# Optimization experiments

Hardware: AMD Instinct MI355X
Metric: run time of the kernel (lower is better)

The kernel has to match this reference:

```python
import jax, jax.numpy as jnp
import numpy as np

NEG_SLOPE = 0.2  # PyG GATConv default negative_slope


def gat_conv(x, edge_index, W, att_src, att_dst, bias):
    """PyG-style GATConv (concat heads, add_self_loops=True, eval mode).
    x: [N, F_in], edge_index: [2, E] (row 0 = src j, row 1 = dst i).
    W: [F_in, H*C], att_src/att_dst: [H, C], bias: [H*C].
    """
    N = x.shape[0]
    H, C = att_src.shape
    loops = jnp.arange(N, dtype=edge_index.dtype)
    src = jnp.concatenate([edge_index[0], loops])  # [E+N]
    dst = jnp.concatenate([edge_index[1], loops])
    h = (x @ W).reshape(N, H, C)                              # [N,H,C]
    a_src = jnp.einsum('nhc,hc->nh', h, att_src)              # [N,H]
    a_dst = jnp.einsum('nhc,hc->nh', h, att_dst)
    alpha = jax.nn.leaky_relu(a_src[src] + a_dst[dst], NEG_SLOPE)  # [E+N,H]
    # segment softmax over edges sharing the same destination node
    m = jax.ops.segment_max(alpha, dst, num_segments=N)       # [N,H]
    e = jnp.exp(alpha - jax.lax.stop_gradient(m)[dst])
    denom = jax.ops.segment_sum(e, dst, num_segments=N)       # [N,H]
    a = e / (denom[dst] + 1e-16)                              # [E+N,H]
    msg = h[src] * a[:, :, None]                              # [E+N,H,C]
    out = jax.ops.segment_sum(msg, dst, num_segments=N)       # [N,H,C]
    return out.reshape(N, H * C) + bias


def setup_inputs() -> dict:
    key = jax.random.key(0)
    ks = jax.random.split(key, 10)
    N, F, NC, C1, H1 = 50000, 128, 40, 16, 8
    E = 800000
    x = jax.random.normal(ks[0], (N, F), dtype=jnp.float32)
    edge_index = jax.random.randint(ks[1], (2, E), 0, N, dtype=jnp.int64)
    s1 = 1.0 / np.sqrt(F)
    W1 = jax.random.uniform(ks[2], (F, H1 * C1), jnp.float32, -s1, s1)
    att_src1 = jax.random.uniform(ks[3], (H1, C1), jnp.float32, -1.0, 1.0) * s1
    att_dst1 = jax.random.uniform(ks[4], (H1, C1), jnp.float32, -1.0, 1.0) * s1
    bias1 = jnp.zeros((H1 * C1,), jnp.float32)
    s2 = 1.0 / np.sqrt(H1 * C1)
    W2 = jax.random.uniform(ks[5], (H1 * C1, NC), jnp.float32, -s2, s2)
    att_src2 = jax.random.uniform(ks[6], (1, NC), jnp.float32, -1.0, 1.0) * s2
    att_dst2 = jax.random.uniform(ks[7], (1, NC), jnp.float32, -1.0, 1.0) * s2
    bias2 = jnp.zeros((NC,), jnp.float32)
    return {"x": x, "edge_index": edge_index, "W1": W1, "att_src1": att_src1,
            "att_dst1": att_dst1, "bias1": bias1, "W2": W2, "att_src2": att_src2,
            "att_dst2": att_dst2, "bias2": bias2}


def reference(x, edge_index, W1, att_src1, att_dst1, bias1, W2, att_src2, att_dst2, bias2):
    h = gat_conv(x, edge_index, W1, att_src1, att_dst1, bias1)   # [N, 128]
    # dropout in eval mode = identity
    out = gat_conv(h, edge_index, W2, att_src2, att_dst2, bias2)  # [N, 40]
    return out
```

## Files before the change

kernel.cpp:

```cpp
#include <hip/hip_runtime.h>
#include <hip/hip_bf16.h>
#include <math.h>

#define NEG_SLOPE 0.2f

typedef __bf16 bf16x8 __attribute__((ext_vector_type(8)));
typedef float f32x4 __attribute__((ext_vector_type(4)));

__device__ __forceinline__ float lrelu(float x) { return x > 0.f ? x : NEG_SLOPE * x; }

__device__ __forceinline__ unsigned short f2bfu(float f) {
    unsigned int ua = __float_as_uint(f);
    return (unsigned short)((ua + 0x7fffu + ((ua >> 16) & 1u)) >> 16);
}
__device__ __forceinline__ float bfu2f(unsigned short u) {
    return __uint_as_float(((unsigned int)u) << 16);
}
__device__ __forceinline__ float bf_lo(unsigned int u) { return __uint_as_float(u << 16); }
__device__ __forceinline__ float bf_hi(unsigned int u) { return __uint_as_float(u & 0xffff0000u); }

__global__ __launch_bounds__(256) void k_hist(const int* __restrict__ ei, int E, int N,
                                              int* __restrict__ cnt, int* __restrict__ rank) {
    int e = blockIdx.x * 256 + threadIdx.x;
    if (e >= E + N) return;
    int d = (e < E) ? ei[E + e] : (e - E);
    rank[e] = atomicAdd(&cnt[d], 1);
}

__global__ __launch_bounds__(256) void k_scan_part(const int* __restrict__ cnt, int N,
                                                   int* __restrict__ psum) {
    __shared__ int sh[256];
    int t = threadIdx.x;
    int base = blockIdx.x * 1024 + t * 4;
    int tl = 0;
#pragma unroll
    for (int j = 0; j < 4; ++j) tl += (base + j < N) ? cnt[base + j] : 0;
    sh[t] = tl; __syncthreads();
    for (int off = 128; off > 0; off >>= 1) {
        if (t < off) sh[t] += sh[t + off];
        __syncthreads();
    }
    if (t == 0) psum[blockIdx.x] = sh[0];
}

__global__ __launch_bounds__(256) void k_scan_mid(int* __restrict__ psum, int nb) {
    __shared__ int sh[256];
    int t = threadIdx.x;
    int v = (t < nb) ? psum[t] : 0;
    sh[t] = v; __syncthreads();
    for (int off = 1; off < 256; off <<= 1) {
        int a = (t >= off) ? sh[t - off] : 0;
        __syncthreads();
        sh[t] += a;
        __syncthreads();
    }
    psum[t] = sh[t] - v;
}

__global__ __launch_bounds__(256) void k_scan_add(const int* __restrict__ cnt, int N,
                                                  const int* __restrict__ psum,
                                                  int* __restrict__ rowptr) {
    __shared__ int sh[256];
    int t = threadIdx.x;
    int base = blockIdx.x * 1024 + t * 4;
    int c[4]; int tl = 0;
#pragma unroll
    for (int j = 0; j < 4; ++j) { c[j] = (base + j < N) ? cnt[base + j] : 0; tl += c[j]; }
    sh[t] = tl; __syncthreads();
    for (int off = 1; off < 256; off <<= 1) {
        int a = (t >= off) ? sh[t - off] : 0;
        __syncthreads();
        sh[t] += a;
        __syncthreads();
    }
    int run = psum[blockIdx.x] + (sh[t] - tl);
#pragma unroll
    for (int j = 0; j < 4; ++j) {
        if (base + j < N) { rowptr[base + j] = run; run += c[j]; }
    }
}

__global__ __launch_bounds__(256) void k_scatter(const int* __restrict__ ei, int E, int N,
                                                 const int* __restrict__ rowptr,
                                                 const int* __restrict__ rank,
                                                 int* __restrict__ col) {
    int e = blockIdx.x * 256 + threadIdx.x;
    if (e >= E + N) return;
    int s, d;
    if (e < E) { s = ei[e]; d = ei[E + e]; } else { s = d = e - E; }
    col[rowptr[d] + rank[e]] = s;
}

__global__ __launch_bounds__(256) void k_wpack(const float* __restrict__ W,
                                               bf16x8* __restrict__ Wp) {
    int idx = blockIdx.x * 256 + threadIdx.x;
    if (idx >= 2048) return;
    int n = idx & 15, quad = (idx >> 4) & 3, c = (idx >> 6) & 3, ct = idx >> 8;
    bf16x8 v;
#pragma unroll
    for (int j = 0; j < 8; ++j)
        v[j] = (__bf16)W[(c * 32 + quad * 8 + j) * 128 + ct * 16 + n];
    Wp[idx] = v;
}

__global__ __launch_bounds__(256) void k_wpack2(const float* __restrict__ W2,
                                                bf16x8* __restrict__ W2p) {
    int idx = blockIdx.x * 256 + threadIdx.x;
    if (idx >= 768) return;
    int n = idx & 15, quad = (idx >> 4) & 3, c = (idx >> 6) & 3, ct = idx >> 8;
    int colc = ct * 16 + n;
    bf16x8 v;
#pragma unroll
    for (int j = 0; j < 8; ++j)
        v[j] = (colc < 40) ? (__bf16)W2[(c * 32 + quad * 8 + j) * 40 + colc] : (__bf16)0.f;
    W2p[idx] = v;
}

__global__ __launch_bounds__(256) void k_gemm1(const float* __restrict__ x,
                                               const bf16x8* __restrict__ Wp,
                                               const float* __restrict__ att_s,
                                               const float* __restrict__ att_d,
                                               unsigned short* __restrict__ h1A,
                                               unsigned short* __restrict__ h1B,
                                               float* __restrict__ a_src,
                                               float* __restrict__ a_dst, int N) {
    int t = threadIdx.x;
    int w = t >> 6, lane = t & 63, quad = lane >> 4, n16 = lane & 15;
    int row0 = blockIdx.x * 64 + w * 16;
    int arow = row0 + n16; if (arow >= N) arow = N - 1;
    const float* px = x + (size_t)arow * 128;

    bf16x8 ah[4], al[4];
#pragma unroll
    for (int c = 0; c < 4; ++c) {
        float4 v0 = *(const float4*)&px[c * 32 + quad * 8];
        float4 v1 = *(const float4*)&px[c * 32 + quad * 8 + 4];
        float xf[8] = {v0.x, v0.y, v0.z, v0.w, v1.x, v1.y, v1.z, v1.w};
#pragma unroll
        for (int j = 0; j < 8; ++j) {
            __bf16 hi = (__bf16)xf[j];
            ah[c][j] = hi;
            al[c][j] = (__bf16)(xf[j] - (float)hi);
        }
    }

    f32x4 acc[8];
#pragma unroll
    for (int ct = 0; ct < 8; ++ct) acc[ct] = (f32x4){0.f, 0.f, 0.f, 0.f};

    const uint4* wp4 = (const uint4*)Wp;
#pragma unroll
    for (int ct = 0; ct < 8; ++ct) {
#pragma unroll
        for (int c = 0; c < 4; ++c) {
            union { uint4 u; bf16x8 b; } bu;
            bu.u = wp4[((ct * 4 + c) * 4 + quad) * 16 + n16];
            acc[ct] = __builtin_amdgcn_mfma_f32_16x16x32_bf16(ah[c], bu.b, acc[ct], 0, 0, 0);
            acc[ct] = __builtin_amdgcn_mfma_f32_16x16x32_bf16(al[c], bu.b, acc[ct], 0, 0, 0);
        }
    }

    float asv[8], adv[8];
#pragma unroll
    for (int ct = 0; ct < 8; ++ct) {
        asv[ct] = att_s[ct * 16 + n16];
        adv[ct] = att_d[ct * 16 + n16];
    }
    int nodeb = row0 + quad * 4;
#pragma unroll
    for (int ct = 0; ct < 8; ++ct) {
        unsigned short* hp = (ct < 4) ? h1A : h1B;
        int chl = (ct & 3) * 16 + n16;
#pragma unroll
        for (int reg = 0; reg < 4; ++reg) {
            int node = nodeb + reg;
            float hv = acc[ct][reg];
            float ps = hv * asv[ct];
            float pd = hv * adv[ct];
#pragma unroll
            for (int m = 1; m < 16; m <<= 1) {
                ps += __shfl_xor(ps, m);
                pd += __shfl_xor(pd, m);
            }
            if (node < N) {
                hp[(size_t)node * 64 + chl] = f2bfu(hv);
                if (n16 == 0) {
                    a_src[(size_t)node * 8 + ct] = ps;
                    a_dst[(size_t)node * 8 + ct] = pd;
                }
            }
        }
    }
}

__global__ __launch_bounds__(256) void k_aggr1(const int* __restrict__ rowptr,
                                               const int* __restrict__ cnt,
                                               const int* __restrict__ col,
                                               const float* __restrict__ a_src,
                                               const float* __restrict__ a_dst,
                                               const unsigned int* __restrict__ hp,
                                               const float* __restrict__ bias1,
                                               unsigned int* __restrict__ out1h,
                                               unsigned int* __restrict__ out1l, int N, int p) {
    __shared__ float evs[4][2][128];
    __shared__ int   cls[4][2][32];
    int t = threadIdx.x;
    int w = t >> 6;
    int lane = t & 63;
    int half = lane >> 5;
    int u = lane & 31;
    int node = blockIdx.x * 8 + w * 2 + half;
    bool nv = (node < N);
    int nodec = nv ? node : (N - 1);
    int beg = rowptr[nodec];
    int deg = nv ? cnt[nodec] : 0;
    int degO = __shfl_xor(deg, 32);
    int degmax = (deg > degO) ? deg : degO;
    if (degmax <= 0) return;

    int hh = u >> 3;
    float4 ad4 = *(const float4*)&a_dst[(size_t)nodec * 8 + p * 4];

    float* myev = &evs[w][half][0];
    int*   mycl = &cls[w][half][0];

    float den = 0.f, n0 = 0.f, n1 = 0.f;
    int c = 0;
    while (c < degmax) {
        int slot = c + u;
        int slotc = (slot < deg) ? slot : (deg - 1);
        if (slotc < 0) slotc = 0;
        int su = col[beg + slotc];
        float4 as4 = *(const float4*)&a_src[(size_t)su * 8 + p * 4];
        bool valid = (slot < deg);
        float e0 = valid ? __expf(lrelu(as4.x + ad4.x)) : 0.f;
        float e1 = valid ? __expf(lrelu(as4.y + ad4.y)) : 0.f;
        float e2 = valid ? __expf(lrelu(as4.z + ad4.z)) : 0.f;
        float e3 = valid ? __expf(lrelu(as4.w + ad4.w)) : 0.f;
        *(float4*)&myev[u * 4] = make_float4(e0, e1, e2, e3);
        mycl[u] = su;

        int ccm = degmax - c; ccm = (ccm < 32) ? ccm : 32;
        int sP = mycl[0];
        unsigned int uP = hp[sP * 32 + u];
        for (int i = 0; i < ccm; ++i) {
            int in = (i + 1 < ccm) ? (i + 1) : i;
            int sN = mycl[in];
            unsigned int uN = hp[sN * 32 + u];
            float ev = myev[i * 4 + hh];
            den += ev;
            n0 = fmaf(ev, bf_lo(uP), n0);
            n1 = fmaf(ev, bf_hi(uP), n1);
            uP = uN;
        }
        c += 32;
    }
    if (nv) {
        float inv = 1.f / (den + 1e-16f);
        int ch = p * 64 + 2 * u;
        float2 b = *(const float2*)&bias1[ch];
        float o0 = fmaf(n0, inv, b.x), o1 = fmaf(n1, inv, b.y);
        unsigned short h0 = f2bfu(o0), h1 = f2bfu(o1);
        float l0 = o0 - bfu2f(h0), l1 = o1 - bfu2f(h1);
        size_t idx = (size_t)node * 64 + p * 32 + u;
        out1h[idx] = (unsigned int)h0 | ((unsigned int)h1 << 16);
        out1l[idx] = (unsigned int)f2bfu(l0) | ((unsigned int)f2bfu(l1) << 16);
    }
}

__global__ __launch_bounds__(256) void k_gemm2(const unsigned int* __restrict__ out1h,
                                               const unsigned int* __restrict__ out1l,
                                               const bf16x8* __restrict__ W2p,
                                               const float* __restrict__ att_s2,
                                               const float* __restrict__ att_d2,
                                               unsigned short* __restrict__ h2s,
                                               float* __restrict__ a_src2,
                                               float* __restrict__ a_dst2, int N) {
    int t = threadIdx.x;
    int w = t >> 6, lane = t & 63, quad = lane >> 4, n16 = lane & 15;
    int row0 = blockIdx.x * 64 + w * 16;
    int arow = row0 + n16; if (arow >= N) arow = N - 1;

    bf16x8 ah[4], al[4];
#pragma unroll
    for (int c = 0; c < 4; ++c) {
        size_t base = (size_t)arow * 64 + (c * 32 + quad * 8) / 2;
        union { uint4 u; bf16x8 b; } hu, lu;
        hu.u = *(const uint4*)&out1h[base];
        lu.u = *(const uint4*)&out1l[base];
        ah[c] = hu.b;
        al[c] = lu.b;
    }

    f32x4 acc[3];
#pragma unroll
    for (int ct = 0; ct < 3; ++ct) acc[ct] = (f32x4){0.f, 0.f, 0.f, 0.f};

    const uint4* wp4 = (const uint4*)W2p;
#pragma unroll
    for (int ct = 0; ct < 3; ++ct) {
#pragma unroll
        for (int c = 0; c < 4; ++c) {
            union { uint4 u; bf16x8 b; } bu;
            bu.u = wp4[((ct * 4 + c) * 4 + quad) * 16 + n16];
            acc[ct] = __builtin_amdgcn_mfma_f32_16x16x32_bf16(ah[c], bu.b, acc[ct], 0, 0, 0);
            acc[ct] = __builtin_amdgcn_mfma_f32_16x16x32_bf16(al[c], bu.b, acc[ct], 0, 0, 0);
        }
    }

    float asv[3], adv[3];
#pragma unroll
    for (int ct = 0; ct < 3; ++ct) {
        int ch = ct * 16 + n16;
        asv[ct] = (ch < 40) ? att_s2[ch] : 0.f;
        adv[ct] = (ch < 40) ? att_d2[ch] : 0.f;
    }
    int nodeb = row0 + quad * 4;
#pragma unroll
    for (int reg = 0; reg < 4; ++reg) {
        int node = nodeb + reg;
        float ps = 0.f, pd = 0.f;
#pragma unroll
        for (int ct = 0; ct < 3; ++ct) {
            float hv = acc[ct][reg];
            ps = fmaf(hv, asv[ct], ps);
            pd = fmaf(hv, adv[ct], pd);
            int ch = ct * 16 + n16;
            if (node < N && ch < 40) h2s[(size_t)node * 40 + ch] = f2bfu(hv);
        }
#pragma unroll
        for (int m = 1; m < 16; m <<= 1) {
            ps += __shfl_xor(ps, m);
            pd += __shfl_xor(pd, m);
        }
        if (node < N && n16 == 0) {
            a_src2[node] = ps;
            a_dst2[node] = pd;
        }
    }
}

__global__ __launch_bounds__(256) void k_aggr2(const int* __restrict__ rowptr,
                                               const int* __restrict__ cnt,
                                               const int* __restrict__ col,
                                               const float* __restrict__ a_src,
                                               const float* __restrict__ a_dst,
                                               const unsigned int* __restrict__ h2b,
                                               const float* __restrict__ bias2,
                                               float* __restrict__ out, int N) {
    __shared__ float evs[4][2][32];
    __shared__ int   cls[4][2][32];
    int t = threadIdx.x;
    int w = t >> 6;
    int lane = t & 63;
    int half = lane >> 5;
    int u = lane & 31;
    int node = blockIdx.x * 8 + w * 2 + half;
    bool nv = (node < N);
    int nodec = nv ? node : (N - 1);
    int beg = rowptr[nodec];
    int deg = nv ? cnt[nodec] : 0;
    int degO = __shfl_xor(deg, 32);
    int degmax = (deg > degO) ? deg : degO;
    if (degmax <= 0) return;

    int ucl = (u < 20) ? u : 19;
    float ad = a_dst[nodec];
    float* myev = &evs[w][half][0];
    int*   mycl = &cls[w][half][0];

    float den = 0.f, a0 = 0.f, a1 = 0.f;
    int c = 0;
    while (c < degmax) {
        int slot = c + u;
        int slotc = (slot < deg) ? slot : (deg - 1);
        if (slotc < 0) slotc = 0;
        int su = col[beg + slotc];
        float ev = (slot < deg) ? __expf(lrelu(a_src[su] + ad)) : 0.f;
        myev[u] = ev;
        mycl[u] = su;

        int ccm = degmax - c; ccm = (ccm < 32) ? ccm : 32;
        int sP = mycl[0];
        unsigned int uP = h2b[sP * 20 + ucl];
        for (int i = 0; i < ccm; ++i) {
            int in = (i + 1 < ccm) ? (i + 1) : i;
            int sN = mycl[in];
            unsigned int uN = h2b[sN * 20 + ucl];
            float evv = myev[i];
            den += evv;
            a0 = fmaf(evv, bf_lo(uP), a0);
            a1 = fmaf(evv, bf_hi(uP), a1);
            uP = uN;
        }
        c += 32;
    }
    if (nv && u < 20) {
        float inv = 1.f / (den + 1e-16f);
        float2 b = *(const float2*)&bias2[2 * u];
        float2 o = make_float2(fmaf(a0, inv, b.x), fmaf(a1, inv, b.y));
        *(float2*)&out[(size_t)node * 40 + 2 * u] = o;
    }
}

extern "C" void kernel_launch(void* const* d_in, const int* in_sizes, int n_in,
                              void* d_out, int out_size, void* d_ws, size_t ws_size,
                              hipStream_t stream) {
    const float* x   = (const float*)d_in[0];
    const int*   ei  = (const int*)d_in[1];
    const float* W1  = (const float*)d_in[2];
    const float* as1 = (const float*)d_in[3];
    const float* ad1 = (const float*)d_in[4];
    const float* b1  = (const float*)d_in[5];
    const float* W2  = (const float*)d_in[6];
    const float* as2 = (const float*)d_in[7];
    const float* ad2 = (const float*)d_in[8];
    const float* b2  = (const float*)d_in[9];

    int N = in_sizes[0] / 128;
    int E = in_sizes[1] / 2;
    int EN = E + N;
    size_t Np = (size_t)((N + 3) & ~3);
    size_t ENp = ((size_t)EN + 3) & ~3;

    float* ws = (float*)d_ws;
    unsigned int* out1h = (unsigned int*)ws; ws += Np * 64;
    unsigned int* out1l = (unsigned int*)ws; ws += Np * 64;
    unsigned int* h1A = (unsigned int*)ws; ws += Np * 32;
    unsigned int* h1Bp = (unsigned int*)ws; ws += Np * 32;
    unsigned int* h2b = (unsigned int*)ws; ws += Np * 20;
    float* a_src1  = ws; ws += Np * 8;
    float* a_dst1  = ws; ws += Np * 8;
    float* a_src2v = ws; ws += Np;
    float* a_dst2v = ws; ws += Np;
    bf16x8* Wp  = (bf16x8*)ws; ws += 2048 * 4;
    bf16x8* W2p = (bf16x8*)ws; ws += 768 * 4;
    int* cnt    = (int*)ws; ws += Np;
    int* rowptr = (int*)ws; ws += Np;
    int* psum   = (int*)ws; ws += 256;
    int* col    = (int*)ws; ws += ENp;
    int* rank   = (int*)ws; ws += ENp;

    int nb = (N + 1023) / 1024;

    hipMemsetAsync(cnt, 0, (size_t)N * sizeof(int), stream);
    k_wpack<<<8, 256, 0, stream>>>(W1, Wp);
    k_wpack2<<<3, 256, 0, stream>>>(W2, W2p);
    k_hist<<<(EN + 255) / 256, 256, 0, stream>>>(ei, E, N, cnt, rank);
    k_scan_part<<<nb, 256, 0, stream>>>(cnt, N, psum);
    k_scan_mid<<<1, 256, 0, stream>>>(psum, nb);
    k_scan_add<<<nb, 256, 0, stream>>>(cnt, N, psum, rowptr);
    k_scatter<<<(EN + 255) / 256, 256, 0, stream>>>(ei, E, N, rowptr, rank, col);

    k_gemm1<<<(N + 63) / 64, 256, 0, stream>>>(x, Wp, as1, ad1,
                                               (unsigned short*)h1A, (unsigned short*)h1Bp,
                                               a_src1, a_dst1, N);
    int nag = (N + 7) / 8;
    k_aggr1<<<nag, 256, 0, stream>>>(rowptr, cnt, col, a_src1, a_dst1, h1A, b1, out1h, out1l, N, 0);
    k_aggr1<<<nag, 256, 0, stream>>>(rowptr, cnt, col, a_src1, a_dst1, h1Bp, b1, out1h, out1l, N, 1);
    k_gemm2<<<(N + 63) / 64, 256, 0, stream>>>(out1h, out1l, W2p, as2, ad2,
                                               (unsigned short*)h2b, a_src2v, a_dst2v, N);
    k_aggr2<<<nag, 256, 0, stream>>>(rowptr, cnt, col, a_src2v, a_dst2v, h2b, b2, (float*)d_out, N);
}
```

Before: 249.4 us.

## Split layer-1 aggregation into four head-pair passes and use 16-bit edge indices

The layer-1 features and source attention scores are stored as four slices of two heads each, 32 channels per slice. Aggregation then runs four passes, each with 16 lanes per destination node instead of two passes with 32 lanes. This shrinks the randomly gathered per-pass working set so it is more likely to stay in cache. The CSR column and rank arrays become 16-bit, halving index traffic, but this only works while the node count and per-node degree stay below 65536. It also adds extra launches and re-reads of the edge list per pass.

```diff
diff --git a/kernel.cpp b/kernel.cpp
--- a/kernel.cpp
+++ b/kernel.cpp
@@ -20,11 +20,12 @@
 __device__ __forceinline__ float bf_hi(unsigned int u) { return __uint_as_float(u & 0xffff0000u); }
 
 __global__ __launch_bounds__(256) void k_hist(const int* __restrict__ ei, int E, int N,
-                                              int* __restrict__ cnt, int* __restrict__ rank) {
+                                              int* __restrict__ cnt,
+                                              unsigned short* __restrict__ rank) {
     int e = blockIdx.x * 256 + threadIdx.x;
     if (e >= E + N) return;
     int d = (e < E) ? ei[E + e] : (e - E);
-    rank[e] = atomicAdd(&cnt[d], 1);
+    rank[e] = (unsigned short)atomicAdd(&cnt[d], 1);
 }
 
 __global__ __launch_bounds__(256) void k_scan_part(const int* __restrict__ cnt, int N,
@@ -82,13 +83,13 @@
 
 __global__ __launch_bounds__(256) void k_scatter(const int* __restrict__ ei, int E, int N,
                                                  const int* __restrict__ rowptr,
-                                                 const int* __restrict__ rank,
-                                                 int* __restrict__ col) {
+                                                 const unsigned short* __restrict__ rank,
+                                                 unsigned short* __restrict__ col) {
     int e = blockIdx.x * 256 + threadIdx.x;
     if (e >= E + N) return;
     int s, d;
     if (e < E) { s = ei[e]; d = ei[E + e]; } else { s = d = e - E; }
-    col[rowptr[d] + rank[e]] = s;
+    col[rowptr[d] + (int)rank[e]] = (unsigned short)s;
 }
 
 __global__ __launch_bounds__(256) void k_wpack(const float* __restrict__ W,
@@ -120,9 +121,8 @@
                                                const bf16x8* __restrict__ Wp,
                                                const float* __restrict__ att_s,
                                                const float* __restrict__ att_d,
-                                               unsigned short* __restrict__ h1A,
-                                               unsigned short* __restrict__ h1B,
-                                               float* __restrict__ a_src,
+                                               unsigned short* __restrict__ h1q, size_t qstride,
+                                               float* __restrict__ a_srcq, size_t astride,
                                                float* __restrict__ a_dst, int N) {
     int t = threadIdx.x;
     int w = t >> 6, lane = t & 63, quad = lane >> 4, n16 = lane & 15;
@@ -169,8 +169,9 @@
     int nodeb = row0 + quad * 4;
 #pragma unroll
     for (int ct = 0; ct < 8; ++ct) {
-        unsigned short* hp = (ct < 4) ? h1A : h1B;
-        int chl = (ct & 3) * 16 + n16;
+        int q = ct >> 1, hsel = ct & 1;
+        unsigned short* hp = h1q + (size_t)q * qstride;
+        int chl = hsel * 16 + n16;
 #pragma unroll
         for (int reg = 0; reg < 4; ++reg) {
             int node = nodeb + reg;
@@ -183,9 +184,9 @@
                 pd += __shfl_xor(pd, m);
             }
             if (node < N) {
-                hp[(size_t)node * 64 + chl] = f2bfu(hv);
+                hp[(size_t)node * 32 + chl] = f2bfu(hv);
                 if (n16 == 0) {
-                    a_src[(size_t)node * 8 + ct] = ps;
+                    a_srcq[(size_t)q * astride + node * 2 + hsel] = ps;
                     a_dst[(size_t)node * 8 + ct] = pd;
                 }
             }
@@ -195,14 +196,160 @@
 
 __global__ __launch_bounds__(256) void k_aggr1(const int* __restrict__ rowptr,
                                                const int* __restrict__ cnt,
-                                               const int* __restrict__ col,
-                                               const float* __restrict__ a_src,
+                                               const unsigned short* __restrict__ col,
+                                               const float* __restrict__ a_srcq,
                                                const float* __restrict__ a_dst,
                                                const unsigned int* __restrict__ hp,
                                                const float* __restrict__ bias1,
                                                unsigned int* __restrict__ out1h,
-                                               unsigned int* __restrict__ out1l, int N, int p) {
-    __shared__ float evs[4][2][128];
+                                               unsigned int* __restrict__ out1l, int N, int q) {
+    __shared__ float evs[4][4][32];
+    __shared__ int   cls[4][4][16];
+    int t = threadIdx.x;
+    int w = t >> 6;
+    int lane = t & 63;
+    int sub = lane >> 4;
+    int u = lane & 15;
+    int node = blockIdx.x * 16 + w * 4 + sub;
+    bool nv = (node < N);
+    int nodec = nv ? node : (N - 1);
+    int beg = rowptr[nodec];
+    int deg = nv ? cnt[nodec] : 0;
+    int m1 = deg, mo;
+    mo = __shfl_xor(m1, 16); m1 = (m1 > mo) ? m1 : mo;
+    mo = __shfl_xor(m1, 32); m1 = (m1 > mo) ? m1 : mo;
+    int degmax = m1;
+    if (degmax <= 0) return;
+
+    int hsel = u >> 3;
+    float2 ad2 = *(const float2*)&a_dst[(size_t)nodec * 8 + q * 2];
+
+    float* myev = &evs[w][sub][0];
+    int*   mycl = &cls[w][sub][0];
+
+    float den = 0.f, n0 = 0.f, n1 = 0.f;
+    int c = 0;
+    while (c < degmax) {
+        int slot = c + u;
+        int slotc = (slot < deg) ? slot : (deg - 1);
+        if (slotc < 0) slotc = 0;
+        int su = (int)col[beg + slotc];
+        float2 as2 = *(const float2*)&a_srcq[(size_t)su * 2];
+        bool valid = (slot < deg);
+        float e0 = valid ? __expf(lrelu(as2.x + ad2.x)) : 0.f;
+        float e1 = valid ? __expf(lrelu(as2.y + ad2.y)) : 0.f;
+        *(float2*)&myev[u * 2] = make_float2(e0, e1);
+        mycl[u] = su;
+
+        int ccm = degmax - c; ccm = (ccm < 16) ? ccm : 16;
+        int sP = mycl[0];
+        unsigned int uP = hp[sP * 16 + u];
+        for (int i = 0; i < ccm; ++i) {
+            int in = (i + 1 < ccm) ? (i + 1) : i;
+            int sN = mycl[in];
+            unsigned int uN = hp[sN * 16 + u];
+            float ev = myev[i * 2 + hsel];
+            den += ev;
+            n0 = fmaf(ev, bf_lo(uP), n0);
+            n1 = fmaf(ev, bf_hi(uP), n1);
+            uP = uN;
+        }
+        c += 16;
+    }
+    if (nv) {
+        float inv = 1.f / (den + 1e-16f);
+        int ch = q * 32 + 2 * u;
+        float2 b = *(const float2*)&bias1[ch];
+        float o0 = fmaf(n0, inv, b.x), o1 = fmaf(n1, inv, b.y);
+        unsigned short h0 = f2bfu(o0), h1 = f2bfu(o1);
+        float l0 = o0 - bfu2f(h0), l1 = o1 - bfu2f(h1);
+        size_t idx = (size_t)node * 64 + q * 16 + u;
+        out1h[idx] = (unsigned int)h0 | ((unsigned int)h1 << 16);
+        out1l[idx] = (unsigned int)f2bfu(l0) | ((unsigned int)f2bfu(l1) << 16);
+    }
+}
+
+__global__ __launch_bounds__(256) void k_gemm2(const unsigned int* __restrict__ out1h,
+                                               const unsigned int* __restrict__ out1l,
+                                               const bf16x8* __restrict__ W2p,
+                                               const float* __restrict__ att_s2,
+                                               const float* __restrict__ att_d2,
+                                               unsigned short* __restrict__ h2s,
+                                               float* __restrict__ a_src2,
+                                               float* __restrict__ a_dst2, int N) {
+    int t = threadIdx.x;
+    int w = t >> 6, lane = t & 63, quad = lane >> 4, n16 = lane & 15;
+    int row0 = blockIdx.x * 64 + w * 16;
+    int arow = row0 + n16; if (arow >= N) arow = N - 1;
+
+    bf16x8 ah[4], al[4];
+#pragma unroll
+    for (int c = 0; c < 4; ++c) {
+        size_t base = (size_t)arow * 64 + (c * 32 + quad * 8) / 2;
+        union { uint4 u; bf16x8 b; } hu, lu;
+        hu.u = *(const uint4*)&out1h[base];
+        lu.u = *(const uint4*)&out1l[base];
+        ah[c] = hu.b;
+        al[c] = lu.b;
+    }
+
+    f32x4 acc[3];
+#pragma unroll
+    for (int ct = 0; ct < 3; ++ct) acc[ct] = (f32x4){0.f, 0.f, 0.f, 0.f};
+
+    const uint4* wp4 = (const uint4*)W2p;
+#pragma unroll
+    for (int ct = 0; ct < 3; ++ct) {
+#pragma unroll
+        for (int c = 0; c < 4; ++c) {
+            union { uint4 u; bf16x8 b; } bu;
+            bu.u = wp4[((ct * 4 + c) * 4 + quad) * 16 + n16];
+            acc[ct] = __builtin_amdgcn_mfma_f32_16x16x32_bf16(ah[c], bu.b, acc[ct], 0, 0, 0);
+            acc[ct] = __builtin_amdgcn_mfma_f32_16x16x32_bf16(al[c], bu.b, acc[ct], 0, 0, 0);
+        }
+    }
+
+    float asv[3], adv[3];
+#pragma unroll
+    for (int ct = 0; ct < 3; ++ct) {
+        int ch = ct * 16 + n16;
+        asv[ct] = (ch < 40) ? att_s2[ch] : 0.f;
+        adv[ct] = (ch < 40) ? att_d2[ch] : 0.f;
+    }
+    int nodeb = row0 + quad * 4;
+#pragma unroll
+    for (int reg = 0; reg < 4; ++reg) {
+        int node = nodeb + reg;
+        float ps = 0.f, pd = 0.f;
+#pragma unroll
+        for (int ct = 0; ct < 3; ++ct) {
+            float hv = acc[ct][reg];
+            ps = fmaf(hv, asv[ct], ps);
+            pd = fmaf(hv, adv[ct], pd);
+            int ch = ct * 16 + n16;
+            if (node < N && ch < 40) h2s[(size_t)node * 40 + ch] = f2bfu(hv);
+        }
+#pragma unroll
+        for (int m = 1; m < 16; m <<= 1) {
+            ps += __shfl_xor(ps, m);
+            pd += __shfl_xor(pd, m);
+        }
+        if (node < N && n16 == 0) {
+            a_src2[node] = ps;
+            a_dst2[node] = pd;
+        }
+    }
+}
+
+__global__ __launch_bounds__(256) void k_aggr2(const int* __restrict__ rowptr,
+                                               const int* __restrict__ cnt,
+                                               const unsigned short* __restrict__ col,
+                                               const float* __restrict__ a_src,
+                                               const float* __restrict__ a_dst,
+                                               const unsigned int* __restrict__ h2b,
+                                               const float* __restrict__ bias2,
+                                               float* __restrict__ out, int N) {
+    __shared__ float evs[4][2][32];
     __shared__ int   cls[4][2][32];
     int t = threadIdx.x;
     int w = t >> 6;
@@ -218,152 +365,6 @@
     int degmax = (deg > degO) ? deg : degO;
     if (degmax <= 0) return;
 
-    int hh = u >> 3;
-    float4 ad4 = *(const float4*)&a_dst[(size_t)nodec * 8 + p * 4];
-
-    float* myev = &evs[w][half][0];
-    int*   mycl = &cls[w][half][0];
-
-    float den = 0.f, n0 = 0.f, n1 = 0.f;
-    int c = 0;
-    while (c < degmax) {
-        int slot = c + u;
-        int slotc = (slot < deg) ? slot : (deg - 1);
-        if (slotc < 0) slotc = 0;
-        int su = col[beg + slotc];
-        float4 as4 = *(const float4*)&a_src[(size_t)su * 8 + p * 4];
-        bool valid = (slot < deg);
-        float e0 = valid ? __expf(lrelu(as4.x + ad4.x)) : 0.f;
-        float e1 = valid ? __expf(lrelu(as4.y + ad4.y)) : 0.f;
-        float e2 = valid ? __expf(lrelu(as4.z + ad4.z)) : 0.f;
-        float e3 = valid ? __expf(lrelu(as4.w + ad4.w)) : 0.f;
-        *(float4*)&myev[u * 4] = make_float4(e0, e1, e2, e3);
-        mycl[u] = su;
-
-        int ccm = degmax - c; ccm = (ccm < 32) ? ccm : 32;
-        int sP = mycl[0];
-        unsigned int uP = hp[sP * 32 + u];
-        for (int i = 0; i < ccm; ++i) {
-            int in = (i + 1 < ccm) ? (i + 1) : i;
-            int sN = mycl[in];
-            unsigned int uN = hp[sN * 32 + u];
-            float ev = myev[i * 4 + hh];
-            den += ev;
-            n0 = fmaf(ev, bf_lo(uP), n0);
-            n1 = fmaf(ev, bf_hi(uP), n1);
-            uP = uN;
-        }
-        c += 32;
-    }
-    if (nv) {
-        float inv = 1.f / (den + 1e-16f);
-        int ch = p * 64 + 2 * u;
-        float2 b = *(const float2*)&bias1[ch];
-        float o0 = fmaf(n0, inv, b.x), o1 = fmaf(n1, inv, b.y);
-        unsigned short h0 = f2bfu(o0), h1 = f2bfu(o1);
-        float l0 = o0 - bfu2f(h0), l1 = o1 - bfu2f(h1);
-        size_t idx = (size_t)node * 64 + p * 32 + u;
-        out1h[idx] = (unsigned int)h0 | ((unsigned int)h1 << 16);
-        out1l[idx] = (unsigned int)f2bfu(l0) | ((unsigned int)f2bfu(l1) << 16);
-    }
-}
-
-__global__ __launch_bounds__(256) void k_gemm2(const unsigned int* __restrict__ out1h,
-                                               const unsigned int* __restrict__ out1l,
-                                               const bf16x8* __restrict__ W2p,
-                                               const float* __restrict__ att_s2,
-                                               const float* __restrict__ att_d2,
-                                               unsigned short* __restrict__ h2s,
-                                               float* __restrict__ a_src2,
-                                               float* __restrict__ a_dst2, int N) {
-    int t = threadIdx.x;
-    int w = t >> 6, lane = t & 63, quad = lane >> 4, n16 = lane & 15;
-    int row0 = blockIdx.x * 64 + w * 16;
-    int arow = row0 + n16; if (arow >= N) arow = N - 1;
-
-    bf16x8 ah[4], al[4];
-#pragma unroll
-    for (int c = 0; c < 4; ++c) {
-        size_t base = (size_t)arow * 64 + (c * 32 + quad * 8) / 2;
-        union { uint4 u; bf16x8 b; } hu, lu;
-        hu.u = *(const uint4*)&out1h[base];
-        lu.u = *(const uint4*)&out1l[base];
-        ah[c] = hu.b;
-        al[c] = lu.b;
-    }
-
-    f32x4 acc[3];
-#pragma unroll
-    for (int ct = 0; ct < 3; ++ct) acc[ct] = (f32x4){0.f, 0.f, 0.f, 0.f};
-
-    const uint4* wp4 = (const uint4*)W2p;
-#pragma unroll
-    for (int ct = 0; ct < 3; ++ct) {
-#pragma unroll
-        for (int c = 0; c < 4; ++c) {
-            union { uint4 u; bf16x8 b; } bu;
-            bu.u = wp4[((ct * 4 + c) * 4 + quad) * 16 + n16];
-            acc[ct] = __builtin_amdgcn_mfma_f32_16x16x32_bf16(ah[c], bu.b, acc[ct], 0, 0, 0);
-            acc[ct] = __builtin_amdgcn_mfma_f32_16x16x32_bf16(al[c], bu.b, acc[ct], 0, 0, 0);
-        }
-    }
-
-    float asv[3], adv[3];
-#pragma unroll
-    for (int ct = 0; ct < 3; ++ct) {
-        int ch = ct * 16 + n16;
-        asv[ct] = (ch < 40) ? att_s2[ch] : 0.f;
-        adv[ct] = (ch < 40) ? att_d2[ch] : 0.f;
-    }
-    int nodeb = row0 + quad * 4;
-#pragma unroll
-    for (int reg = 0; reg < 4; ++reg) {
-        int node = nodeb + reg;
-        float ps = 0.f, pd = 0.f;
-#pragma unroll
-        for (int ct = 0; ct < 3; ++ct) {
-            float hv = acc[ct][reg];
-            ps = fmaf(hv, asv[ct], ps);
-            pd = fmaf(hv, adv[ct], pd);
-            int ch = ct * 16 + n16;
-            if (node < N && ch < 40) h2s[(size_t)node * 40 + ch] = f2bfu(hv);
-        }
-#pragma unroll
-        for (int m = 1; m < 16; m <<= 1) {
-            ps += __shfl_xor(ps, m);
-            pd += __shfl_xor(pd, m);
-        }
-        if (node < N && n16 == 0) {
-            a_src2[node] = ps;
-            a_dst2[node] = pd;
-        }
-    }
-}
-
-__global__ __launch_bounds__(256) void k_aggr2(const int* __restrict__ rowptr,
-                                               const int* __restrict__ cnt,
-                                               const int* __restrict__ col,
-                                               const float* __restrict__ a_src,
-                                               const float* __restrict__ a_dst,
-                                               const unsigned int* __restrict__ h2b,
-                                               const float* __restrict__ bias2,
-                                               float* __restrict__ out, int N) {
-    __shared__ float evs[4][2][32];
-    __shared__ int   cls[4][2][32];
-    int t = threadIdx.x;
-    int w = t >> 6;
-    int lane = t & 63;
-    int half = lane >> 5;
-    int u = lane & 31;
-    int node = blockIdx.x * 8 + w * 2 + half;
-    bool nv = (node < N);
-    int nodec = nv ? node : (N - 1);
-    int beg = rowptr[nodec];
-    int deg = nv ? cnt[nodec] : 0;
-    int degO = __shfl_xor(deg, 32);
-    int degmax = (deg > degO) ? deg : degO;
-    if (degmax <= 0) return;
-
     int ucl = (u < 20) ? u : 19;
     float ad = a_dst[nodec];
     float* myev = &evs[w][half][0];
@@ -375,7 +376,7 @@
         int slot = c + u;
         int slotc = (slot < deg) ? slot : (deg - 1);
         if (slotc < 0) slotc = 0;
-        int su = col[beg + slotc];
+        int su = (int)col[beg + slotc];
         float ev = (slot < deg) ? __expf(lrelu(a_src[su] + ad)) : 0.f;
         myev[u] = ev;
         mycl[u] = su;
@@ -426,10 +427,9 @@
     float* ws = (float*)d_ws;
     unsigned int* out1h = (unsigned int*)ws; ws += Np * 64;
     unsigned int* out1l = (unsigned int*)ws; ws += Np * 64;
-    unsigned int* h1A = (unsigned int*)ws; ws += Np * 32;
-    unsigned int* h1Bp = (unsigned int*)ws; ws += Np * 32;
+    unsigned short* h1q = (unsigned short*)ws; ws += Np * 64;
     unsigned int* h2b = (unsigned int*)ws; ws += Np * 20;
-    float* a_src1  = ws; ws += Np * 8;
+    float* a_srcq  = ws; ws += Np * 8;
     float* a_dst1  = ws; ws += Np * 8;
     float* a_src2v = ws; ws += Np;
     float* a_dst2v = ws; ws += Np;
@@ -438,8 +438,11 @@
     int* cnt    = (int*)ws; ws += Np;
     int* rowptr = (int*)ws; ws += Np;
     int* psum   = (int*)ws; ws += 256;
-    int* col    = (int*)ws; ws += ENp;
-    int* rank   = (int*)ws; ws += ENp;
+    unsigned short* col  = (unsigned short*)ws; ws += ENp / 2 + 4;
+    unsigned short* rank = (unsigned short*)ws; ws += ENp / 2 + 4;
+
+    size_t qstride = Np * 32;
+    size_t astride = Np * 2;
 
     int nb = (N + 1023) / 1024;
 
@@ -452,13 +455,16 @@
     k_scan_add<<<nb, 256, 0, stream>>>(cnt, N, psum, rowptr);
     k_scatter<<<(EN + 255) / 256, 256, 0, stream>>>(ei, E, N, rowptr, rank, col);
 
-    k_gemm1<<<(N + 63) / 64, 256, 0, stream>>>(x, Wp, as1, ad1,
-                                               (unsigned short*)h1A, (unsigned short*)h1Bp,
-                                               a_src1, a_dst1, N);
-    int nag = (N + 7) / 8;
-    k_aggr1<<<nag, 256, 0, stream>>>(rowptr, cnt, col, a_src1, a_dst1, h1A, b1, out1h, out1l, N, 0);
-    k_aggr1<<<nag, 256, 0, stream>>>(rowptr, cnt, col, a_src1, a_dst1, h1Bp, b1, out1h, out1l, N, 1);
+    k_gemm1<<<(N + 63) / 64, 256, 0, stream>>>(x, Wp, as1, ad1, h1q, qstride,
+                                               a_srcq, astride, a_dst1, N);
+    int nag1 = (N + 15) / 16;
+    for (int q = 0; q < 4; ++q)
+        k_aggr1<<<nag1, 256, 0, stream>>>(rowptr, cnt, col,
+                                          a_srcq + (size_t)q * astride, a_dst1,
+                                          (const unsigned int*)(h1q + (size_t)q * qstride),
+                                          b1, out1h, out1l, N, q);
     k_gemm2<<<(N + 63) / 64, 256, 0, stream>>>(out1h, out1l, W2p, as2, ad2,
                                                (unsigned short*)h2b, a_src2v, a_dst2v, N);
-    k_aggr2<<<nag, 256, 0, stream>>>(rowptr, cnt, col, a_src2v, a_dst2v, h2b, b2, (float*)d_out, N);
-}
+    int nag2 = (N + 7) / 8;
+    k_aggr2<<<nag2, 256, 0, stream>>>(rowptr, cnt, col, a_src2v, a_dst2v, h2b, b2, (float*)d_out, N);
+}
```

Result: slower. 272.3 us (+9.2%).

## Merge preprocessing launches, single-block scan, and 16-bit column/rank indices

Applied to the files above, without the earlier changes.

Fuses the two weight-packing kernels and the count memset into one prep kernel, and replaces the three-kernel prefix scan with a single 1024-thread block scan. Column and rank arrays are narrowed to unsigned 16-bit, which halves index traffic in scatter and the aggregation gathers. This relies on N and per-node degree fitting in 16 bits (N=50000 fits), so it breaks for larger graphs. The single-block scan serialises ~49 elements per thread, which may be slower than the multi-block version.

```diff
diff --git a/kernel.cpp b/kernel.cpp
--- a/kernel.cpp
+++ b/kernel.cpp
@@ -19,101 +19,70 @@
 __device__ __forceinline__ float bf_lo(unsigned int u) { return __uint_as_float(u << 16); }
 __device__ __forceinline__ float bf_hi(unsigned int u) { return __uint_as_float(u & 0xffff0000u); }
 
+__global__ __launch_bounds__(256) void k_prep(const float* __restrict__ W1,
+                                              bf16x8* __restrict__ Wp,
+                                              const float* __restrict__ W2,
+                                              bf16x8* __restrict__ W2p,
+                                              int* __restrict__ cnt, int N) {
+    int g = blockIdx.x * 256 + threadIdx.x;
+    if (g < 2048) {
+        int n = g & 15, quad = (g >> 4) & 3, c = (g >> 6) & 3, ct = g >> 8;
+        bf16x8 v;
+#pragma unroll
+        for (int j = 0; j < 8; ++j)
+            v[j] = (__bf16)W1[(c * 32 + quad * 8 + j) * 128 + ct * 16 + n];
+        Wp[g] = v;
+    } else if (g < 2816) {
+        int idx = g - 2048;
+        int n = idx & 15, quad = (idx >> 4) & 3, c = (idx >> 6) & 3, ct = idx >> 8;
+        int colc = ct * 16 + n;
+        bf16x8 v;
+#pragma unroll
+        for (int j = 0; j < 8; ++j)
+            v[j] = (colc < 40) ? (__bf16)W2[(c * 32 + quad * 8 + j) * 40 + colc] : (__bf16)0.f;
+        W2p[idx] = v;
+    }
+    if (g < N) cnt[g] = 0;
+}
+
 __global__ __launch_bounds__(256) void k_hist(const int* __restrict__ ei, int E, int N,
-                                              int* __restrict__ cnt, int* __restrict__ rank) {
+                                              int* __restrict__ cnt,
+                                              unsigned short* __restrict__ rank) {
     int e = blockIdx.x * 256 + threadIdx.x;
     if (e >= E + N) return;
     int d = (e < E) ? ei[E + e] : (e - E);
-    rank[e] = atomicAdd(&cnt[d], 1);
-}
-
-__global__ __launch_bounds__(256) void k_scan_part(const int* __restrict__ cnt, int N,
-                                                   int* __restrict__ psum) {
-    __shared__ int sh[256];
+    rank[e] = (unsigned short)atomicAdd(&cnt[d], 1);
+}
+
+__global__ __launch_bounds__(1024) void k_scan(const int* __restrict__ cnt, int N,
+                                               int* __restrict__ rowptr) {
+    __shared__ int sh[1024];
     int t = threadIdx.x;
-    int base = blockIdx.x * 1024 + t * 4;
-    int tl = 0;
-#pragma unroll
-    for (int j = 0; j < 4; ++j) tl += (base + j < N) ? cnt[base + j] : 0;
-    sh[t] = tl; __syncthreads();
-    for (int off = 128; off > 0; off >>= 1) {
-        if (t < off) sh[t] += sh[t + off];
+    int chunk = (N + 1023) >> 10;
+    int lo = t * chunk;
+    int hi = lo + chunk; if (hi > N) hi = N;
+    int s = 0;
+    for (int i = lo; i < hi; ++i) s += cnt[i];
+    sh[t] = s; __syncthreads();
+    for (int off = 1; off < 1024; off <<= 1) {
+        int v = (t >= off) ? sh[t - off] : 0;
         __syncthreads();
-    }
-    if (t == 0) psum[blockIdx.x] = sh[0];
-}
-
-__global__ __launch_bounds__(256) void k_scan_mid(int* __restrict__ psum, int nb) {
-    __shared__ int sh[256];
-    int t = threadIdx.x;
-    int v = (t < nb) ? psum[t] : 0;
-    sh[t] = v; __syncthreads();
-    for (int off = 1; off < 256; off <<= 1) {
-        int a = (t >= off) ? sh[t - off] : 0;
+        sh[t] += v;
         __syncthreads();
-        sh[t] += a;
-        __syncthreads();
-    }
-    psum[t] = sh[t] - v;
-}
-
-__global__ __launch_bounds__(256) void k_scan_add(const int* __restrict__ cnt, int N,
-                                                  const int* __restrict__ psum,
-                                                  int* __restrict__ rowptr) {
-    __shared__ int sh[256];
-    int t = threadIdx.x;
-    int base = blockIdx.x * 1024 + t * 4;
-    int c[4]; int tl = 0;
-#pragma unroll
-    for (int j = 0; j < 4; ++j) { c[j] = (base + j < N) ? cnt[base + j] : 0; tl += c[j]; }
-    sh[t] = tl; __syncthreads();
-    for (int off = 1; off < 256; off <<= 1) {
-        int a = (t >= off) ? sh[t - off] : 0;
-        __syncthreads();
-        sh[t] += a;
-        __syncthreads();
-    }
-    int run = psum[blockIdx.x] + (sh[t] - tl);
-#pragma unroll
-    for (int j = 0; j < 4; ++j) {
-        if (base + j < N) { rowptr[base + j] = run; run += c[j]; }
-    }
+    }
+    int run = sh[t] - s;
+    for (int i = lo; i < hi; ++i) { rowptr[i] = run; run += cnt[i]; }
 }
 
 __global__ __launch_bounds__(256) void k_scatter(const int* __restrict__ ei, int E, int N,
                                                  const int* __restrict__ rowptr,
-                                                 const int* __restrict__ rank,
-                                                 int* __restrict__ col) {
+                                                 const unsigned short* __restrict__ rank,
+                                                 unsigned short* __restrict__ col) {
     int e = blockIdx.x * 256 + threadIdx.x;
     if (e >= E + N) return;
     int s, d;
     if (e < E) { s = ei[e]; d = ei[E + e]; } else { s = d = e - E; }
-    col[rowptr[d] + rank[e]] = s;
-}
-
-__global__ __launch_bounds__(256) void k_wpack(const float* __restrict__ W,
-                                               bf16x8* __restrict__ Wp) {
-    int idx = blockIdx.x * 256 + threadIdx.x;
-    if (idx >= 2048) return;
-    int n = idx & 15, quad = (idx >> 4) & 3, c = (idx >> 6) & 3, ct = idx >> 8;
-    bf16x8 v;
-#pragma unroll
-    for (int j = 0; j < 8; ++j)
-        v[j] = (__bf16)W[(c * 32 + quad * 8 + j) * 128 + ct * 16 + n];
-    Wp[idx] = v;
-}
-
-__global__ __launch_bounds__(256) void k_wpack2(const float* __restrict__ W2,
-                                                bf16x8* __restrict__ W2p) {
-    int idx = blockIdx.x * 256 + threadIdx.x;
-    if (idx >= 768) return;
-    int n = idx & 15, quad = (idx >> 4) & 3, c = (idx >> 6) & 3, ct = idx >> 8;
-    int colc = ct * 16 + n;
-    bf16x8 v;
-#pragma unroll
-    for (int j = 0; j < 8; ++j)
-        v[j] = (colc < 40) ? (__bf16)W2[(c * 32 + quad * 8 + j) * 40 + colc] : (__bf16)0.f;
-    W2p[idx] = v;
+    col[rowptr[d] + (int)rank[e]] = (unsigned short)s;
 }
 
 __global__ __launch_bounds__(256) void k_gemm1(const float* __restrict__ x,
@@ -195,7 +164,7 @@
 
 __global__ __launch_bounds__(256) void k_aggr1(const int* __restrict__ rowptr,
                                                const int* __restrict__ cnt,
-                                               const int* __restrict__ col,
+                                               const unsigned short* __restrict__ col,
                                                const float* __restrict__ a_src,
                                                const float* __restrict__ a_dst,
                                                const unsigned int* __restrict__ hp,
@@ -230,7 +199,7 @@
         int slot = c + u;
         int slotc = (slot < deg) ? slot : (deg - 1);
         if (slotc < 0) slotc = 0;
-        int su = col[beg + slotc];
+        int su = (int)col[beg + slotc];
         float4 as4 = *(const float4*)&a_src[(size_t)su * 8 + p * 4];
         bool valid = (slot < deg);
         float e0 = valid ? __expf(lrelu(as4.x + ad4.x)) : 0.f;
@@ -342,7 +311,7 @@
 
 __global__ __launch_bounds__(256) void k_aggr2(const int* __restrict__ rowptr,
                                                const int* __restrict__ cnt,
-                                               const int* __restrict__ col,
+                                               const unsigned short* __restrict__ col,
                                                const float* __restrict__ a_src,
                                                const float* __restrict__ a_dst,
                                                const unsigned int* __restrict__ h2b,
@@ -375,7 +344,7 @@
         int slot = c + u;
         int slotc = (slot < deg) ? slot : (deg - 1);
         if (slotc < 0) slotc = 0;
-        int su = col[beg + slotc];
+        int su = (int)col[beg + slotc];
         float ev = (slot < deg) ? __expf(lrelu(a_src[su] + ad)) : 0.f;
         myev[u] = ev;
         mycl[u] = su;
@@ -437,19 +406,13 @@
     bf16x8* W2p = (bf16x8*)ws; ws += 768 * 4;
     int* cnt    = (int*)ws; ws += Np;
     int* rowptr = (int*)ws; ws += Np;
-    int* psum   = (int*)ws; ws += 256;
-    int* col    = (int*)ws; ws += ENp;
-    int* rank   = (int*)ws; ws += ENp;
-
-    int nb = (N + 1023) / 1024;
-
-    hipMemsetAsync(cnt, 0, (size_t)N * sizeof(int), stream);
-    k_wpack<<<8, 256, 0, stream>>>(W1, Wp);
-    k_wpack2<<<3, 256, 0, stream>>>(W2, W2p);
+    unsigned short* col  = (unsigned short*)ws; ws += ENp / 2 + 4;
+    unsigned short* rank = (unsigned short*)ws; ws += ENp / 2 + 4;
+
+    int npre = (N > 2816 ? N : 2816);
+    k_prep<<<(npre + 255) / 256, 256, 0, stream>>>(W1, Wp, W2, W2p, cnt, N);
     k_hist<<<(EN + 255) / 256, 256, 0, stream>>>(ei, E, N, cnt, rank);
-    k_scan_part<<<nb, 256, 0, stream>>>(cnt, N, psum);
-    k_scan_mid<<<1, 256, 0, stream>>>(psum, nb);
-    k_scan_add<<<nb, 256, 0, stream>>>(cnt, N, psum, rowptr);
+    k_scan<<<1, 1024, 0, stream>>>(cnt, N, rowptr);
     k_scatter<<<(EN + 255) / 256, 256, 0, stream>>>(ei, E, N, rowptr, rank, col);
 
     k_gemm1<<<(N + 63) / 64, 256, 0, stream>>>(x, Wp, as1, ad1,
```

After: 312.0 us. 1.25x slower.
